# Kernel optimization log

Measured on AMD Instinct MI355X. Metric: run time of the kernel, lower is better.

## Reference

```python
import jax, jax.numpy as jnp
import numpy as np

EPS = 1e-5

def layer_norm(x, gamma, beta):
    m = jnp.mean(x, axis=-1, keepdims=True)
    v = jnp.var(x, axis=-1, keepdims=True)
    return (x - m) * jax.lax.rsqrt(v + EPS) * gamma + beta


def setup_inputs() -> dict:
    key = jax.random.key(0)
    ks = jax.random.split(key, 8)
    B, N, E, C = 1, 512, 128, 128
    s = 0.02
    inp = {
        "pair_rep": jax.random.normal(ks[0], (B, N, N, E), dtype=jnp.float32),
        "ln_pair_g": jnp.ones((E,), jnp.float32),
        "ln_pair_b": jnp.zeros((E,), jnp.float32),
        "ga_w": jax.random.normal(ks[1], (E, C), jnp.float32) * s,
        "ga_b": jnp.zeros((C,), jnp.float32),
        "la_w": jax.random.normal(ks[2], (E, C), jnp.float32) * s,
        "la_b": jnp.zeros((C,), jnp.float32),
        "gb_w": jax.random.normal(ks[3], (E, C), jnp.float32) * s,
        "gb_b": jnp.zeros((C,), jnp.float32),
        "lb_w": jax.random.normal(ks[4], (E, C), jnp.float32) * s,
        "lb_b": jnp.zeros((C,), jnp.float32),
        "g_w": jax.random.normal(ks[5], (E, E), jnp.float32) * s,
        "g_b": jnp.zeros((E,), jnp.float32),
        "ln_up_g": jnp.ones((C,), jnp.float32),
        "ln_up_b": jnp.zeros((C,), jnp.float32),
        "lu_w": jax.random.normal(ks[6], (C, E), jnp.float32) * s,
        "lu_b": jnp.zeros((E,), jnp.float32),
    }
    return inp


def reference(pair_rep, ln_pair_g, ln_pair_b, ga_w, ga_b, la_w, la_b,
              gb_w, gb_b, lb_w, lb_b, g_w, g_b, ln_up_g, ln_up_b, lu_w, lu_b):
    # pair_rep: [B, N, N, E]
    z = layer_norm(pair_rep, ln_pair_g, ln_pair_b)
    a = jax.nn.sigmoid(z @ ga_w + ga_b) * (z @ la_w + la_b)  # [B,N,N,C]
    b = jax.nn.sigmoid(z @ gb_w + gb_b) * (z @ lb_w + lb_b)  # [B,N,N,C]
    g = jax.nn.sigmoid(z @ g_w + g_b)                        # [B,N,N,E]
    # torch: sum(a.unsqueeze(-3)*b.unsqueeze(-4), dim=-2) == sum_k a[i,k,c]*b[j,k,c]
    update = jnp.einsum("bikc,bjkc->bijc", a, b)             # [B,N,N,C]
    out = g * (layer_norm(update, ln_up_g, ln_up_b) @ lu_w + lu_b)
    return out
```

## Files before the change

### kernel.cpp

```cpp
#include <hip/hip_runtime.h>
#include <hip/hip_bf16.h>

#define NN 512
#define MM (NN*NN)

typedef __attribute__((ext_vector_type(8))) unsigned short u16x8;
typedef __attribute__((ext_vector_type(4))) unsigned short u16x4;
typedef __attribute__((ext_vector_type(8))) __bf16 bf16x8;
typedef __attribute__((ext_vector_type(4))) float f32x4;

static __device__ __forceinline__ unsigned short f2bf(float f) {
  unsigned int u = __float_as_uint(f);
  u = (u + 0x7FFFu + ((u >> 16) & 1u)) >> 16;
  return (unsigned short)u;
}
static __device__ __forceinline__ float bf2f(unsigned short h) {
  return __uint_as_float(((unsigned int)h) << 16);
}
static __device__ __forceinline__ bf16x8 ldfrag(const unsigned short* p) {
  u16x8 v = *(const u16x8*)p;
  return __builtin_bit_cast(bf16x8, v);
}
static __device__ __forceinline__ float sigm(float x) {
  return 1.0f / (1.0f + __expf(-x));
}

__global__ void prep_weights(const float* __restrict__ ga_w, const float* __restrict__ la_w,
                             const float* __restrict__ gb_w, const float* __restrict__ lb_w,
                             const float* __restrict__ g_w,  const float* __restrict__ lu_w,
                             unsigned short* __restrict__ WT) {
  int idx = blockIdx.x * 256 + threadIdx.x;
  if (idx >= 768 * 128) return;
  int n = idx >> 7;
  int k = idx & 127;
  int grp = n >> 7, cn = n & 127;
  const float* tabs[6] = {ga_w, la_w, gb_w, lb_w, g_w, lu_w};
  WT[idx] = f2bf(tabs[grp][k * 128 + cn]);
}

__global__ __launch_bounds__(512, 4) void k1_proj(
    const float* __restrict__ pair, const float* __restrict__ lng, const float* __restrict__ lnb,
    const unsigned short* __restrict__ WT,
    const float* __restrict__ ga_b, const float* __restrict__ la_b,
    const float* __restrict__ gb_b, const float* __restrict__ lb_b,
    const float* __restrict__ g_b,
    unsigned short* __restrict__ a_t, unsigned short* __restrict__ b_t,
    unsigned short* __restrict__ g_buf) {
  __shared__ __align__(16) unsigned short sA[128 * 136];
  __shared__ __align__(16) unsigned short sB[128 * 136];
  const int t = threadIdx.x;
  const size_t m0 = (size_t)blockIdx.x * 128;

  {
    const int row = t >> 2, q = t & 3;
    const float* pr = pair + (m0 + row) * 128 + q * 32;
    float vals[32];
    float s = 0.f, ss = 0.f;
#pragma unroll
    for (int it = 0; it < 8; ++it) {
      f32x4 v = *(const f32x4*)(pr + it * 4);
#pragma unroll
      for (int j = 0; j < 4; ++j) { float x = v[j]; vals[it * 4 + j] = x; s += x; ss += x * x; }
    }
    s += __shfl_xor(s, 1);  s += __shfl_xor(s, 2);
    ss += __shfl_xor(ss, 1); ss += __shfl_xor(ss, 2);
    const float mean = s * (1.f / 128.f);
    const float var  = ss * (1.f / 128.f) - mean * mean;
    const float rstd = rsqrtf(var + 1e-5f);
#pragma unroll
    for (int i = 0; i < 4; ++i) {
      u16x8 pk;
#pragma unroll
      for (int j = 0; j < 8; ++j) {
        int c = q * 32 + i * 8 + j;
        pk[j] = f2bf((vals[i * 8 + j] - mean) * rstd * lng[c] + lnb[c]);
      }
      *(u16x8*)(sA + row * 136 + q * 32 + i * 8) = pk;
    }
  }
  __syncthreads();

  const int wave = t >> 6, lane = t & 63, lrow = lane & 15, qk = lane >> 4;

  bf16x8 af[4];
#pragma unroll
  for (int ks = 0; ks < 4; ++ks)
    af[ks] = ldfrag(sA + (wave * 16 + lrow) * 136 + ks * 32 + 8 * qk);

  f32x4 accg[8], accl[8];

  for (int pass = 0; pass < 2; ++pass) {
#pragma unroll
    for (int sub = 0; sub < 2; ++sub) {
      __syncthreads();
      const int base = pass * 256 + sub * 128;
#pragma unroll
      for (int it = 0; it < 4; ++it) {
        int idx = it * 512 + t;
        int n = idx >> 4, off = (idx & 15) * 8;
        *(u16x8*)(sB + n * 136 + off) = *(const u16x8*)(WT + (size_t)(base + n) * 128 + off);
      }
      __syncthreads();
      f32x4* acc = sub ? accl : accg;
#pragma unroll
      for (int nt = 0; nt < 8; ++nt)
#pragma unroll
        for (int r = 0; r < 4; ++r) acc[nt][r] = 0.f;
#pragma unroll
      for (int ks = 0; ks < 4; ++ks) {
#pragma unroll
        for (int nt = 0; nt < 8; ++nt) {
          bf16x8 bv = ldfrag(sB + (nt * 16 + lrow) * 136 + ks * 32 + 8 * qk);
          acc[nt] = __builtin_amdgcn_mfma_f32_16x16x32_bf16(af[ks], bv, acc[nt], 0, 0, 0);
        }
      }
    }
    __syncthreads();
    {
      const float* gbias = (pass == 0) ? ga_b : gb_b;
      const float* lbias = (pass == 0) ? la_b : lb_b;
#pragma unroll
      for (int nt = 0; nt < 8; ++nt) {
        int col = nt * 16 + lrow;
        float bg = gbias[col], bl = lbias[col];
        u16x4 pk;
#pragma unroll
        for (int r = 0; r < 4; ++r)
          pk[r] = f2bf(sigm(accg[nt][r] + bg) * (accl[nt][r] + bl));
        *(u16x4*)(sB + col * 136 + wave * 16 + qk * 4) = pk;
      }
    }
    __syncthreads();
    {
      unsigned short* dst = (pass == 0) ? a_t : b_t;
#pragma unroll
      for (int it = 0; it < 4; ++it) {
        int idx = it * 512 + t;
        int col = idx >> 4, i = idx & 15;
        *(u16x8*)(dst + (size_t)col * MM + m0 + i * 8) = *(const u16x8*)(sB + col * 136 + i * 8);
      }
    }
  }

  __syncthreads();
#pragma unroll
  for (int it = 0; it < 4; ++it) {
    int idx = it * 512 + t;
    int n = idx >> 4, off = (idx & 15) * 8;
    *(u16x8*)(sB + n * 136 + off) = *(const u16x8*)(WT + (size_t)(512 + n) * 128 + off);
  }
  __syncthreads();
#pragma unroll
  for (int nt = 0; nt < 8; ++nt)
#pragma unroll
    for (int r = 0; r < 4; ++r) accg[nt][r] = 0.f;
#pragma unroll
  for (int ks = 0; ks < 4; ++ks) {
#pragma unroll
    for (int nt = 0; nt < 8; ++nt) {
      bf16x8 bv = ldfrag(sB + (nt * 16 + lrow) * 136 + ks * 32 + 8 * qk);
      accg[nt] = __builtin_amdgcn_mfma_f32_16x16x32_bf16(af[ks], bv, accg[nt], 0, 0, 0);
    }
  }
  __syncthreads();
#pragma unroll
  for (int nt = 0; nt < 8; ++nt) {
    int col = nt * 16 + lrow;
    float bg = g_b[col];
#pragma unroll
    for (int r = 0; r < 4; ++r)
      sB[(wave * 16 + qk * 4 + r) * 136 + col] = f2bf(sigm(accg[nt][r] + bg));
  }
  __syncthreads();
#pragma unroll
  for (int it = 0; it < 4; ++it) {
    int idx = it * 512 + t;
    int mr = idx >> 4, off = (idx & 15) * 8;
    *(u16x8*)(g_buf + (m0 + mr) * 128 + off) = *(const u16x8*)(sB + mr * 136 + off);
  }
}

__global__ __launch_bounds__(256) void k2_einsum(
    const unsigned short* __restrict__ a_t, const unsigned short* __restrict__ b_t,
    unsigned short* __restrict__ up_t) {
  __shared__ __align__(16) unsigned short sA[128 * 40];
  __shared__ __align__(16) unsigned short sB[128 * 40];
  const int t = threadIdx.x;
  const int c = blockIdx.y;
  const int i0 = (blockIdx.x >> 2) * 128, j0 = (blockIdx.x & 3) * 128;
  const unsigned short* Ag = a_t + (size_t)c * MM + (size_t)i0 * 512;
  const unsigned short* Bg = b_t + (size_t)c * MM + (size_t)j0 * 512;
  const int wave = t >> 6, lane = t & 63, wr = wave >> 1, wc = wave & 1;
  const int lrow = lane & 15, qk = lane >> 4;
  f32x4 acc[4][4];
#pragma unroll
  for (int i = 0; i < 4; ++i)
#pragma unroll
    for (int j = 0; j < 4; ++j)
#pragma unroll
      for (int r = 0; r < 4; ++r) acc[i][j][r] = 0.f;

  for (int ks = 0; ks < 16; ++ks) {
    const int k0 = ks * 32;
#pragma unroll
    for (int h = 0; h < 2; ++h) {
      int idx = h * 256 + t;
      int row = idx >> 2, qq = idx & 3;
      *(u16x8*)(sA + row * 40 + qq * 8) = *(const u16x8*)(Ag + (size_t)row * 512 + k0 + qq * 8);
      *(u16x8*)(sB + row * 40 + qq * 8) = *(const u16x8*)(Bg + (size_t)row * 512 + k0 + qq * 8);
    }
    __syncthreads();
    bf16x8 af[4], bv[4];
#pragma unroll
    for (int mt = 0; mt < 4; ++mt)
      af[mt] = ldfrag(sA + (wr * 64 + mt * 16 + lrow) * 40 + 8 * qk);
#pragma unroll
    for (int nt = 0; nt < 4; ++nt)
      bv[nt] = ldfrag(sB + (wc * 64 + nt * 16 + lrow) * 40 + 8 * qk);
#pragma unroll
    for (int mt = 0; mt < 4; ++mt)
#pragma unroll
      for (int nt = 0; nt < 4; ++nt)
        acc[mt][nt] = __builtin_amdgcn_mfma_f32_16x16x32_bf16(af[mt], bv[nt], acc[mt][nt], 0, 0, 0);
    __syncthreads();
  }
  unsigned short* up = up_t + (size_t)c * MM;
#pragma unroll
  for (int mt = 0; mt < 4; ++mt)
#pragma unroll
    for (int nt = 0; nt < 4; ++nt) {
      int col = j0 + wc * 64 + nt * 16 + lrow;
#pragma unroll
      for (int r = 0; r < 4; ++r) {
        int row = i0 + wr * 64 + mt * 16 + qk * 4 + r;
        up[(size_t)row * 512 + col] = f2bf(acc[mt][nt][r]);
      }
    }
}

__global__ __launch_bounds__(256) void k3_final(
    const unsigned short* __restrict__ up_t, const unsigned short* __restrict__ g_buf,
    const unsigned short* __restrict__ WT,
    const float* __restrict__ lnug, const float* __restrict__ lnub,
    const float* __restrict__ lu_b, float* __restrict__ out) {
  __shared__ __align__(16) unsigned short sU[64 * 138];
  __shared__ __align__(16) unsigned short sA[64 * 136];
  __shared__ __align__(16) unsigned short sB[128 * 136];
  const int t = threadIdx.x;
  const size_t m0 = (size_t)blockIdx.x * 64;
#pragma unroll
  for (int it = 0; it < 4; ++it) {
    int idx = it * 256 + t;
    int c = idx >> 3, m8 = (idx & 7) * 8;
    u16x8 v = *(const u16x8*)(up_t + (size_t)c * MM + m0 + m8);
#pragma unroll
    for (int j = 0; j < 8; ++j) sU[(m8 + j) * 138 + c] = v[j];
  }
#pragma unroll
  for (int it = 0; it < 8; ++it) {
    int idx = it * 256 + t;
    int n = idx >> 4, off = (idx & 15) * 8;
    *(u16x8*)(sB + n * 136 + off) = *(const u16x8*)(WT + (size_t)(640 + n) * 128 + off);
  }
  __syncthreads();
  {
    const int row = t >> 2, q = t & 3;
    float vals[32]; float s = 0.f, ss = 0.f;
#pragma unroll
    for (int jj = 0; jj < 32; ++jj) {
      int cc = q + jj * 4;
      float x = bf2f(sU[row * 138 + cc]);
      vals[jj] = x; s += x; ss += x * x;
    }
    s += __shfl_xor(s, 1);  s += __shfl_xor(s, 2);
    ss += __shfl_xor(ss, 1); ss += __shfl_xor(ss, 2);
    float mean = s * (1.f / 128.f);
    float var  = ss * (1.f / 128.f) - mean * mean;
    float rstd = rsqrtf(var + 1e-5f);
#pragma unroll
    for (int jj = 0; jj < 32; ++jj) {
      int cc = q + jj * 4;
      float zn = (vals[jj] - mean) * rstd * lnug[cc] + lnub[cc];
      sA[row * 136 + cc] = f2bf(zn);
    }
  }
  __syncthreads();
  const int wave = t >> 6, lane = t & 63, lrow = lane & 15, qk = lane >> 4;
  f32x4 acc[8];
#pragma unroll
  for (int i = 0; i < 8; ++i)
#pragma unroll
    for (int r = 0; r < 4; ++r) acc[i][r] = 0.f;
#pragma unroll
  for (int ks = 0; ks < 4; ++ks) {
    int k0 = ks * 32;
    bf16x8 af = ldfrag(sA + (wave * 16 + lrow) * 136 + k0 + 8 * qk);
#pragma unroll
    for (int nt = 0; nt < 8; ++nt) {
      bf16x8 bv = ldfrag(sB + (nt * 16 + lrow) * 136 + k0 + 8 * qk);
      acc[nt] = __builtin_amdgcn_mfma_f32_16x16x32_bf16(af, bv, acc[nt], 0, 0, 0);
    }
  }
#pragma unroll
  for (int nt = 0; nt < 8; ++nt) {
    int e = nt * 16 + lrow;
    float bb = lu_b[e];
#pragma unroll
    for (int r = 0; r < 4; ++r) {
      size_t m = m0 + wave * 16 + qk * 4 + r;
      float lin = acc[nt][r] + bb;
      float gv = bf2f(g_buf[m * 128 + e]);
      out[m * 128 + e] = gv * lin;
    }
  }
}

extern "C" void kernel_launch(void* const* d_in, const int* in_sizes, int n_in,
                              void* d_out, int out_size, void* d_ws, size_t ws_size,
                              hipStream_t stream) {
  const float* pair = (const float*)d_in[0];
  const float* lng  = (const float*)d_in[1];
  const float* lnb  = (const float*)d_in[2];
  const float* ga_w = (const float*)d_in[3];
  const float* ga_b = (const float*)d_in[4];
  const float* la_w = (const float*)d_in[5];
  const float* la_b = (const float*)d_in[6];
  const float* gb_w = (const float*)d_in[7];
  const float* gb_b = (const float*)d_in[8];
  const float* lb_w = (const float*)d_in[9];
  const float* lb_b = (const float*)d_in[10];
  const float* g_w  = (const float*)d_in[11];
  const float* g_b  = (const float*)d_in[12];
  const float* lnug = (const float*)d_in[13];
  const float* lnub = (const float*)d_in[14];
  const float* lu_w = (const float*)d_in[15];
  const float* lu_b = (const float*)d_in[16];
  float* out = (float*)d_out;

  char* ws = (char*)d_ws;
  unsigned short* WT    = (unsigned short*)(ws);
  unsigned short* a_t   = (unsigned short*)(ws + 196608ull);
  unsigned short* b_t   = (unsigned short*)(ws + 67305472ull);
  unsigned short* g_buf = (unsigned short*)(ws + 134414336ull);
  unsigned short* up_t  = (unsigned short*)(ws + 201523200ull);

  hipLaunchKernelGGL(prep_weights, dim3(384), dim3(256), 0, stream,
                     ga_w, la_w, gb_w, lb_w, g_w, lu_w, WT);
  hipLaunchKernelGGL(k1_proj, dim3(2048), dim3(512), 0, stream,
                     pair, lng, lnb, WT, ga_b, la_b, gb_b, lb_b, g_b, a_t, b_t, g_buf);
  hipLaunchKernelGGL(k2_einsum, dim3(16, 128), dim3(256), 0, stream, a_t, b_t, up_t);
  hipLaunchKernelGGL(k3_final, dim3(4096), dim3(256), 0, stream,
                     up_t, g_buf, WT, lnug, lnub, lu_b, out);
}
```

Baseline: 315.2 us.

## Pipeline weight staging in projection kernel and double-buffer einsum tiles

The projection kernel now prefetches the next weight slab into registers while the current GEMM runs, using two LDS buffers in place of load-sync-compute rounds. The g output is written straight to global memory from registers, dropping one LDS round trip. The einsum kernel double-buffers its LDS tiles with register prefetch, cutting one barrier per k-step, and remaps block indices so blocks sharing a channel are spread across XCDs. The conversion to bf16 now uses the HIP intrinsic. In exchange, register pressure rises and the direct g_buf stores are uncoalesced scalar writes.

```diff
diff --git a/kernel.cpp b/kernel.cpp
--- a/kernel.cpp
+++ b/kernel.cpp
@@ -9,10 +9,8 @@
 typedef __attribute__((ext_vector_type(8))) __bf16 bf16x8;
 typedef __attribute__((ext_vector_type(4))) float f32x4;
 
-static __device__ __forceinline__ unsigned short f2bf(float f) {
-  unsigned int u = __float_as_uint(f);
-  u = (u + 0x7FFFu + ((u >> 16) & 1u)) >> 16;
-  return (unsigned short)u;
+static __device__ __forceinline__ unsigned short f2bfi(float f) {
+  return __builtin_bit_cast(unsigned short, __float2bfloat16(f));
 }
 static __device__ __forceinline__ float bf2f(unsigned short h) {
   return __uint_as_float(((unsigned int)h) << 16);
@@ -35,7 +33,7 @@
   int k = idx & 127;
   int grp = n >> 7, cn = n & 127;
   const float* tabs[6] = {ga_w, la_w, gb_w, lb_w, g_w, lu_w};
-  WT[idx] = f2bf(tabs[grp][k * 128 + cn]);
+  WT[idx] = f2bfi(tabs[grp][k * 128 + cn]);
 }
 
 __global__ __launch_bounds__(512, 4) void k1_proj(
@@ -46,10 +44,27 @@
     const float* __restrict__ g_b,
     unsigned short* __restrict__ a_t, unsigned short* __restrict__ b_t,
     unsigned short* __restrict__ g_buf) {
-  __shared__ __align__(16) unsigned short sA[128 * 136];
-  __shared__ __align__(16) unsigned short sB[128 * 136];
+  __shared__ __align__(16) unsigned short W0[128 * 136];
+  __shared__ __align__(16) unsigned short W1[128 * 136];
   const int t = threadIdx.x;
   const size_t m0 = (size_t)blockIdx.x * 128;
+  const int wave = t >> 6, lane = t & 63, lrow = lane & 15, qk = lane >> 4;
+  const int rbase = t >> 4, off_ = (t & 15) * 8;
+
+  u16x8 rga[4], rla[4], rgb[4], rlb[4], rg[4];
+  auto stage_ld = [&](u16x8* r, int base) {
+#pragma unroll
+    for (int it = 0; it < 4; ++it)
+      r[it] = *(const u16x8*)(WT + (size_t)(base + it * 32 + rbase) * 128 + off_);
+  };
+  auto stage_st = [&](unsigned short* buf, const u16x8* r) {
+#pragma unroll
+    for (int it = 0; it < 4; ++it)
+      *(u16x8*)(buf + (it * 32 + rbase) * 136 + off_) = r[it];
+  };
+
+  stage_ld(rga, 0);
+  stage_ld(rla, 128);
 
   {
     const int row = t >> 2, q = t & 3;
@@ -73,125 +88,101 @@
 #pragma unroll
       for (int j = 0; j < 8; ++j) {
         int c = q * 32 + i * 8 + j;
-        pk[j] = f2bf((vals[i * 8 + j] - mean) * rstd * lng[c] + lnb[c]);
+        pk[j] = f2bfi((vals[i * 8 + j] - mean) * rstd * lng[c] + lnb[c]);
       }
-      *(u16x8*)(sA + row * 136 + q * 32 + i * 8) = pk;
-    }
-  }
-  __syncthreads();
-
-  const int wave = t >> 6, lane = t & 63, lrow = lane & 15, qk = lane >> 4;
+      *(u16x8*)(W0 + row * 136 + q * 32 + i * 8) = pk;
+    }
+  }
+  __syncthreads();
 
   bf16x8 af[4];
+  f32x4 accg[8], accl[8];
+  auto run_gemm = [&](const unsigned short* buf, f32x4* acc) {
+#pragma unroll
+    for (int nt = 0; nt < 8; ++nt)
+#pragma unroll
+      for (int r = 0; r < 4; ++r) acc[nt][r] = 0.f;
+#pragma unroll
+    for (int ks = 0; ks < 4; ++ks)
+#pragma unroll
+      for (int nt = 0; nt < 8; ++nt) {
+        bf16x8 bv = ldfrag(buf + (nt * 16 + lrow) * 136 + ks * 32 + 8 * qk);
+        acc[nt] = __builtin_amdgcn_mfma_f32_16x16x32_bf16(af[ks], bv, acc[nt], 0, 0, 0);
+      }
+  };
+  auto epi_ab = [&](unsigned short* buf, const float* gbias, const float* lbias) {
+#pragma unroll
+    for (int nt = 0; nt < 8; ++nt) {
+      int col = nt * 16 + lrow;
+      float bg = gbias[col], bl = lbias[col];
+      u16x4 pk;
+#pragma unroll
+      for (int r = 0; r < 4; ++r)
+        pk[r] = f2bfi(sigm(accg[nt][r] + bg) * (accl[nt][r] + bl));
+      *(u16x4*)(buf + col * 136 + wave * 16 + qk * 4) = pk;
+    }
+  };
+  auto wout = [&](unsigned short* dst, const unsigned short* buf) {
+#pragma unroll
+    for (int it = 0; it < 4; ++it) {
+      int idx = it * 512 + t;
+      int col = idx >> 4, i = idx & 15;
+      *(u16x8*)(dst + (size_t)col * MM + m0 + i * 8) = *(const u16x8*)(buf + col * 136 + i * 8);
+    }
+  };
+
 #pragma unroll
   for (int ks = 0; ks < 4; ++ks)
-    af[ks] = ldfrag(sA + (wave * 16 + lrow) * 136 + ks * 32 + 8 * qk);
-
-  f32x4 accg[8], accl[8];
-
-  for (int pass = 0; pass < 2; ++pass) {
-#pragma unroll
-    for (int sub = 0; sub < 2; ++sub) {
-      __syncthreads();
-      const int base = pass * 256 + sub * 128;
-#pragma unroll
-      for (int it = 0; it < 4; ++it) {
-        int idx = it * 512 + t;
-        int n = idx >> 4, off = (idx & 15) * 8;
-        *(u16x8*)(sB + n * 136 + off) = *(const u16x8*)(WT + (size_t)(base + n) * 128 + off);
-      }
-      __syncthreads();
-      f32x4* acc = sub ? accl : accg;
-#pragma unroll
-      for (int nt = 0; nt < 8; ++nt)
-#pragma unroll
-        for (int r = 0; r < 4; ++r) acc[nt][r] = 0.f;
-#pragma unroll
-      for (int ks = 0; ks < 4; ++ks) {
-#pragma unroll
-        for (int nt = 0; nt < 8; ++nt) {
-          bf16x8 bv = ldfrag(sB + (nt * 16 + lrow) * 136 + ks * 32 + 8 * qk);
-          acc[nt] = __builtin_amdgcn_mfma_f32_16x16x32_bf16(af[ks], bv, acc[nt], 0, 0, 0);
-        }
-      }
-    }
-    __syncthreads();
-    {
-      const float* gbias = (pass == 0) ? ga_b : gb_b;
-      const float* lbias = (pass == 0) ? la_b : lb_b;
-#pragma unroll
-      for (int nt = 0; nt < 8; ++nt) {
-        int col = nt * 16 + lrow;
-        float bg = gbias[col], bl = lbias[col];
-        u16x4 pk;
-#pragma unroll
-        for (int r = 0; r < 4; ++r)
-          pk[r] = f2bf(sigm(accg[nt][r] + bg) * (accl[nt][r] + bl));
-        *(u16x4*)(sB + col * 136 + wave * 16 + qk * 4) = pk;
-      }
-    }
-    __syncthreads();
-    {
-      unsigned short* dst = (pass == 0) ? a_t : b_t;
-#pragma unroll
-      for (int it = 0; it < 4; ++it) {
-        int idx = it * 512 + t;
-        int col = idx >> 4, i = idx & 15;
-        *(u16x8*)(dst + (size_t)col * MM + m0 + i * 8) = *(const u16x8*)(sB + col * 136 + i * 8);
-      }
-    }
-  }
-
-  __syncthreads();
-#pragma unroll
-  for (int it = 0; it < 4; ++it) {
-    int idx = it * 512 + t;
-    int n = idx >> 4, off = (idx & 15) * 8;
-    *(u16x8*)(sB + n * 136 + off) = *(const u16x8*)(WT + (size_t)(512 + n) * 128 + off);
-  }
-  __syncthreads();
-#pragma unroll
-  for (int nt = 0; nt < 8; ++nt)
-#pragma unroll
-    for (int r = 0; r < 4; ++r) accg[nt][r] = 0.f;
-#pragma unroll
-  for (int ks = 0; ks < 4; ++ks) {
-#pragma unroll
-    for (int nt = 0; nt < 8; ++nt) {
-      bf16x8 bv = ldfrag(sB + (nt * 16 + lrow) * 136 + ks * 32 + 8 * qk);
-      accg[nt] = __builtin_amdgcn_mfma_f32_16x16x32_bf16(af[ks], bv, accg[nt], 0, 0, 0);
-    }
-  }
-  __syncthreads();
+    af[ks] = ldfrag(W0 + (wave * 16 + lrow) * 136 + ks * 32 + 8 * qk);
+  stage_st(W1, rga);
+  stage_ld(rgb, 256);
+  __syncthreads();
+  run_gemm(W1, accg);
+  stage_st(W0, rla);
+  stage_ld(rlb, 384);
+  __syncthreads();
+  run_gemm(W0, accl);
+  stage_st(W1, rgb);
+  stage_ld(rg, 512);
+  __syncthreads();
+  epi_ab(W0, ga_b, la_b);
+  __syncthreads();
+  wout(a_t, W0);
+  run_gemm(W1, accg);
+  __syncthreads();
+  stage_st(W0, rlb);
+  stage_st(W1, rg);
+  __syncthreads();
+  run_gemm(W0, accl);
+  __syncthreads();
+  epi_ab(W0, gb_b, lb_b);
+  run_gemm(W1, accg);
+  __syncthreads();
+  wout(b_t, W0);
 #pragma unroll
   for (int nt = 0; nt < 8; ++nt) {
     int col = nt * 16 + lrow;
     float bg = g_b[col];
 #pragma unroll
     for (int r = 0; r < 4; ++r)
-      sB[(wave * 16 + qk * 4 + r) * 136 + col] = f2bf(sigm(accg[nt][r] + bg));
-  }
-  __syncthreads();
-#pragma unroll
-  for (int it = 0; it < 4; ++it) {
-    int idx = it * 512 + t;
-    int mr = idx >> 4, off = (idx & 15) * 8;
-    *(u16x8*)(g_buf + (m0 + mr) * 128 + off) = *(const u16x8*)(sB + mr * 136 + off);
+      g_buf[(m0 + wave * 16 + qk * 4 + r) * 128 + col] = f2bfi(sigm(accg[nt][r] + bg));
   }
 }
 
 __global__ __launch_bounds__(256) void k2_einsum(
     const unsigned short* __restrict__ a_t, const unsigned short* __restrict__ b_t,
     unsigned short* __restrict__ up_t) {
-  __shared__ __align__(16) unsigned short sA[128 * 40];
-  __shared__ __align__(16) unsigned short sB[128 * 40];
+  __shared__ __align__(16) unsigned short sA[2][128 * 40];
+  __shared__ __align__(16) unsigned short sB[2][128 * 40];
   const int t = threadIdx.x;
-  const int c = blockIdx.y;
-  const int i0 = (blockIdx.x >> 2) * 128, j0 = (blockIdx.x & 3) * 128;
+  const int wid = (blockIdx.x & 7) * 256 + (blockIdx.x >> 3);
+  const int c = wid >> 4;
+  const int i0 = ((wid >> 2) & 3) * 128, j0 = (wid & 3) * 128;
   const unsigned short* Ag = a_t + (size_t)c * MM + (size_t)i0 * 512;
   const unsigned short* Bg = b_t + (size_t)c * MM + (size_t)j0 * 512;
   const int wave = t >> 6, lane = t & 63, wr = wave >> 1, wc = wave & 1;
   const int lrow = lane & 15, qk = lane >> 4;
+  const int srow = t >> 2, sq = t & 3;
   f32x4 acc[4][4];
 #pragma unroll
   for (int i = 0; i < 4; ++i)
@@ -200,29 +191,45 @@
 #pragma unroll
       for (int r = 0; r < 4; ++r) acc[i][j][r] = 0.f;
 
+  u16x8 ra[2], rb[2];
+  auto tile_ld = [&](int k0) {
+#pragma unroll
+    for (int h = 0; h < 2; ++h) {
+      int row = h * 64 + srow;
+      ra[h] = *(const u16x8*)(Ag + (size_t)row * 512 + k0 + sq * 8);
+      rb[h] = *(const u16x8*)(Bg + (size_t)row * 512 + k0 + sq * 8);
+    }
+  };
+  auto tile_st = [&](int buf) {
+#pragma unroll
+    for (int h = 0; h < 2; ++h) {
+      int row = h * 64 + srow;
+      *(u16x8*)(sA[buf] + row * 40 + sq * 8) = ra[h];
+      *(u16x8*)(sB[buf] + row * 40 + sq * 8) = rb[h];
+    }
+  };
+
+  tile_ld(0);
+  tile_st(0);
+  __syncthreads();
+  int cur = 0;
   for (int ks = 0; ks < 16; ++ks) {
-    const int k0 = ks * 32;
-#pragma unroll
-    for (int h = 0; h < 2; ++h) {
-      int idx = h * 256 + t;
-      int row = idx >> 2, qq = idx & 3;
-      *(u16x8*)(sA + row * 40 + qq * 8) = *(const u16x8*)(Ag + (size_t)row * 512 + k0 + qq * 8);
-      *(u16x8*)(sB + row * 40 + qq * 8) = *(const u16x8*)(Bg + (size_t)row * 512 + k0 + qq * 8);
-    }
+    if (ks < 15) tile_ld((ks + 1) * 32);
+    bf16x8 afr[4], bv[4];
+#pragma unroll
+    for (int mt = 0; mt < 4; ++mt)
+      afr[mt] = ldfrag(sA[cur] + (wr * 64 + mt * 16 + lrow) * 40 + 8 * qk);
+#pragma unroll
+    for (int nt = 0; nt < 4; ++nt)
+      bv[nt] = ldfrag(sB[cur] + (wc * 64 + nt * 16 + lrow) * 40 + 8 * qk);
+#pragma unroll
+    for (int mt = 0; mt < 4; ++mt)
+#pragma unroll
+      for (int nt = 0; nt < 4; ++nt)
+        acc[mt][nt] = __builtin_amdgcn_mfma_f32_16x16x32_bf16(afr[mt], bv[nt], acc[mt][nt], 0, 0, 0);
+    if (ks < 15) tile_st(cur ^ 1);
     __syncthreads();
-    bf16x8 af[4], bv[4];
-#pragma unroll
-    for (int mt = 0; mt < 4; ++mt)
-      af[mt] = ldfrag(sA + (wr * 64 + mt * 16 + lrow) * 40 + 8 * qk);
-#pragma unroll
-    for (int nt = 0; nt < 4; ++nt)
-      bv[nt] = ldfrag(sB + (wc * 64 + nt * 16 + lrow) * 40 + 8 * qk);
-#pragma unroll
-    for (int mt = 0; mt < 4; ++mt)
-#pragma unroll
-      for (int nt = 0; nt < 4; ++nt)
-        acc[mt][nt] = __builtin_amdgcn_mfma_f32_16x16x32_bf16(af[mt], bv[nt], acc[mt][nt], 0, 0, 0);
-    __syncthreads();
+    cur ^= 1;
   }
   unsigned short* up = up_t + (size_t)c * MM;
 #pragma unroll
@@ -233,7 +240,7 @@
 #pragma unroll
       for (int r = 0; r < 4; ++r) {
         int row = i0 + wr * 64 + mt * 16 + qk * 4 + r;
-        up[(size_t)row * 512 + col] = f2bf(acc[mt][nt][r]);
+        up[(size_t)row * 512 + col] = f2bfi(acc[mt][nt][r]);
       }
     }
 }
@@ -281,7 +288,7 @@
     for (int jj = 0; jj < 32; ++jj) {
       int cc = q + jj * 4;
       float zn = (vals[jj] - mean) * rstd * lnug[cc] + lnub[cc];
-      sA[row * 136 + cc] = f2bf(zn);
+      sA[row * 136 + cc] = f2bfi(zn);
     }
   }
   __syncthreads();
@@ -348,7 +355,7 @@
                      ga_w, la_w, gb_w, lb_w, g_w, lu_w, WT);
   hipLaunchKernelGGL(k1_proj, dim3(2048), dim3(512), 0, stream,
                      pair, lng, lnb, WT, ga_b, la_b, gb_b, lb_b, g_b, a_t, b_t, g_buf);
-  hipLaunchKernelGGL(k2_einsum, dim3(16, 128), dim3(256), 0, stream, a_t, b_t, up_t);
+  hipLaunchKernelGGL(k2_einsum, dim3(2048), dim3(256), 0, stream, a_t, b_t, up_t);
   hipLaunchKernelGGL(k3_final, dim3(4096), dim3(256), 0, stream,
                      up_t, g_buf, WT, lnug, lnub, lu_b, out);
 }
```

Result: faster. 297.7 us (-5.5%).
